# Performance work log

Measured on AMD Instinct MI355X. Metric: run time of the kernel, lower is better.

The kernel has to match this reference:

```python
import jax, jax.numpy as jnp
import numpy as np

B, T, D, H = 4, 2048, 1024, 16
HD = D // H  # 64


def setup_inputs() -> dict:
    key = jax.random.key(0)
    ks = jax.random.split(key, 5)
    return {
        "x": jax.random.normal(ks[0], (B, T, D), dtype=jnp.float32),
        "W_qkv": jax.random.normal(ks[1], (D, 3 * D), dtype=jnp.float32) * 0.02,
        "b_qkv": jax.random.normal(ks[2], (3 * D,), dtype=jnp.float32) * 0.02,
        "W_out": jax.random.normal(ks[3], (D, D), dtype=jnp.float32) * 0.02,
        "b_out": jax.random.normal(ks[4], (D,), dtype=jnp.float32) * 0.02,
        "mask": 1,
    }


def reference(x, W_qkv, b_qkv, W_out, b_out, mask):
    # fused QKV projection: (B,T,3D)
    qkv = x @ W_qkv + b_qkv
    # torch layout: view (B,T,H,3*hd) then chunk last dim into q,k,v
    qkv = qkv.reshape(B, T, H, 3, HD)
    q = qkv[..., 0, :].transpose(0, 2, 1, 3)  # (B,H,T,hd)
    k = qkv[..., 1, :].transpose(0, 2, 1, 3)
    v = qkv[..., 2, :].transpose(0, 2, 1, 3)
    scores = jnp.einsum('bhqd,bhkd->bhqk', q, k) / jnp.sqrt(jnp.float32(HD))
    if mask:
        causal = jnp.triu(jnp.ones((T, T), dtype=bool), k=1)
        scores = jnp.where(causal[None, None], jnp.float32(-jnp.inf), scores)
    attn = jax.nn.softmax(scores, axis=-1)
    out = jnp.einsum('bhqk,bhkd->bhqd', attn, v)  # (B,H,T,hd)
    out = out.transpose(0, 2, 1, 3).reshape(B, T, D)
    return out @ W_out + b_out
```

## Files before the change

### kernel.cpp

```cpp
#include <hip/hip_runtime.h>

typedef unsigned short u16;
typedef __bf16 bf16x8 __attribute__((ext_vector_type(8)));
typedef float f32x4 __attribute__((ext_vector_type(4)));
typedef float f32x16 __attribute__((ext_vector_type(16)));

#define DEV __device__ __forceinline__

constexpr int Bb = 4, Tt = 2048, Dd = 1024, Hh = 16, HDd = 64;
constexpr int MM = Bb * Tt;
constexpr float QSCALE = 0.125f * 1.4426950408889634f;

DEV u16 f2bf(float f) {
  unsigned u = __float_as_uint(f);
  u += 0x7fffu + ((u >> 16) & 1u);
  return (u16)(u >> 16);
}

DEV unsigned cvtpk(float a, float b) {
  unsigned r;
  asm("v_cvt_pk_bf16_f32 %0, %1, %2" : "=v"(r) : "v"(a), "v"(b));
  return r;
}

DEV void pswap(unsigned& a, unsigned& b) {
  asm("v_permlane32_swap_b32 %0, %1" : "+v"(a), "+v"(b));
}

DEV void gload_lds16(const u16* g, u16* l) {
  __builtin_amdgcn_global_load_lds(
      (const __attribute__((address_space(1))) void*)g,
      (__attribute__((address_space(3))) void*)l, 16, 0, 0);
}

__global__ __launch_bounds__(256) void cast_x_kernel(const float* __restrict__ in,
                                                     u16* __restrict__ out, int n8) {
  int i = blockIdx.x * 256 + threadIdx.x;
  if (i >= n8) return;
  const float4* p = (const float4*)in + (size_t)i * 2;
  float4 v0 = p[0], v1 = p[1];
  union { u16 u[8]; uint4 v; } t;
  t.u[0] = f2bf(v0.x); t.u[1] = f2bf(v0.y); t.u[2] = f2bf(v0.z); t.u[3] = f2bf(v0.w);
  t.u[4] = f2bf(v1.x); t.u[5] = f2bf(v1.y); t.u[6] = f2bf(v1.z); t.u[7] = f2bf(v1.w);
  ((uint4*)out)[i] = t.v;
}

__global__ __launch_bounds__(256) void wcast_t_kernel(const float* __restrict__ in,
                                                      u16* __restrict__ out, int K, int N) {
  __shared__ float tile[32][33];
  int n0 = blockIdx.x * 32, k0 = blockIdx.y * 32;
  int tx = threadIdx.x & 31, ty = threadIdx.x >> 5;
  #pragma unroll
  for (int yy = ty; yy < 32; yy += 8)
    tile[yy][tx] = in[(size_t)(k0 + yy) * N + n0 + tx];
  __syncthreads();
  #pragma unroll
  for (int yy = ty; yy < 32; yy += 8)
    out[(size_t)(n0 + yy) * K + k0 + tx] = f2bf(tile[tx][yy]);
}

DEV void stage_tile(const u16* __restrict__ src, int row0, int k0, int ld, u16* lds) {
  int t = threadIdx.x, w = t >> 6;
  #pragma unroll
  for (int j = 0; j < 2; ++j) {
    int e = (j * 256 + t) * 8;
    int r = e >> 5;
    int slot = (e >> 3) & 3;
    int c = (slot ^ ((r >> 1) & 3)) << 3;
    gload_lds16(src + (size_t)(row0 + r) * ld + k0 + c, lds + j * 2048 + w * 512);
  }
}

template <int EPI>
__global__ __launch_bounds__(256) void gemm_bt_kernel(
    const u16* __restrict__ A, const u16* __restrict__ Bt,
    const float* __restrict__ bias, float* __restrict__ Cf,
    u16* __restrict__ Qb, u16* __restrict__ Kb, u16* __restrict__ Vtb,
    int M, int N, int Kd) {
  __shared__ __align__(16) u16 SH[24576];
  int nx = N >> 7;
  int bid = blockIdx.y * nx + blockIdx.x;
  int nwg = (M >> 7) * nx;
  int swz = (bid & 7) * (nwg >> 3) + (bid >> 3);
  int m0 = (swz / nx) * 128, n0 = (swz % nx) * 128;

  int tid = threadIdx.x, l = tid & 63, w = tid >> 6;
  int lo = l & 15, g = l >> 4;
  int wm = (w >> 1) * 64, wn = (w & 1) * 64;
  f32x4 acc[4][4] = {};
  int nk = Kd >> 5;
  stage_tile(A, m0, 0, Kd, SH);
  stage_tile(Bt, n0, 0, Kd, SH + 12288);
  stage_tile(A, m0, 32, Kd, SH + 4096);
  stage_tile(Bt, n0, 32, Kd, SH + 12288 + 4096);
  asm volatile("s_waitcnt vmcnt(4)" ::: "memory");
  __builtin_amdgcn_s_barrier();
  for (int kt = 0; kt < nk; ++kt) {
    if (kt + 2 < nk) {
      int bi = (kt + 2) % 3;
      stage_tile(A, m0, (kt + 2) * 32, Kd, SH + bi * 4096);
      stage_tile(Bt, n0, (kt + 2) * 32, Kd, SH + 12288 + bi * 4096);
    }
    const u16* Ac = SH + (kt % 3) * 4096;
    const u16* Bc = SH + 12288 + (kt % 3) * 4096;
    bf16x8 a[4], b[4];
    #pragma unroll
    for (int i = 0; i < 4; ++i) {
      int row = wm + i * 16 + lo;
      a[i] = *(const bf16x8*)&Ac[row * 32 + ((g ^ ((row >> 1) & 3)) << 3)];
    }
    #pragma unroll
    for (int j = 0; j < 4; ++j) {
      int row = wn + j * 16 + lo;
      b[j] = *(const bf16x8*)&Bc[row * 32 + ((g ^ ((row >> 1) & 3)) << 3)];
    }
    #pragma unroll
    for (int i = 0; i < 4; ++i)
      #pragma unroll
      for (int j = 0; j < 4; ++j)
        acc[i][j] = __builtin_amdgcn_mfma_f32_16x16x32_bf16(a[i], b[j], acc[i][j], 0, 0, 0);
    if (kt + 2 < nk) {
      asm volatile("s_waitcnt vmcnt(4)" ::: "memory");
    } else {
      asm volatile("s_waitcnt vmcnt(0)" ::: "memory");
    }
    __builtin_amdgcn_s_barrier();
  }
  if (EPI == 0) {
    u16* ep = SH + w * 4096;
    int nblk = n0 + wn;
    int hh = nblk / 192, which = (nblk % 192) >> 6;
    int mblk = m0 + wm;
    int b_ = mblk >> 11, t0 = mblk & (Tt - 1);
    if (which == 2) {
      #pragma unroll
      for (int j = 0; j < 4; ++j) {
        float bv = bias[nblk + j * 16 + lo];
        int rowp = j * 16 + lo;
        #pragma unroll
        for (int i = 0; i < 4; ++i) {
          int slotp = i * 2 + (g >> 1);
          #pragma unroll
          for (int r = 0; r < 4; ++r) {
            ep[rowp * 64 + ((slotp ^ (rowp & 7)) << 3) + (g & 1) * 4 + r] =
                f2bf(acc[i][j][r] + bv);
          }
        }
      }
      asm volatile("s_waitcnt lgkmcnt(0)" ::: "memory");
      u16* dst = Vtb + (size_t)(b_ * Hh + hh) * HDd * Tt + t0;
      #pragma unroll
      for (int s = 0; s < 8; ++s) {
        int row = s * 8 + (l >> 3);
        int phys = ((l & 7) ^ (row & 7)) << 3;
        uint4 v = *(const uint4*)&ep[row * 64 + phys];
        *(uint4*)(dst + (size_t)row * Tt + (l & 7) * 8) = v;
      }
    } else {
      float qs = (which == 0) ? QSCALE : 1.0f;
      #pragma unroll
      for (int j = 0; j < 4; ++j) {
        float bv = bias[nblk + j * 16 + lo];
        int slot = j * 2 + (lo >> 3);
        #pragma unroll
        for (int i = 0; i < 4; ++i) {
          #pragma unroll
          for (int r = 0; r < 4; ++r) {
            int lrow = i * 16 + g * 4 + r;
            ep[lrow * 64 + ((slot ^ (lrow & 7)) << 3) + (lo & 7)] =
                f2bf((acc[i][j][r] + bv) * qs);
          }
        }
      }
      asm volatile("s_waitcnt lgkmcnt(0)" ::: "memory");
      u16* dst = (which == 0) ? Qb : Kb;
      dst += ((size_t)(b_ * Hh + hh) * Tt + t0) * HDd;
      #pragma unroll
      for (int s = 0; s < 8; ++s) {
        int row = s * 8 + (l >> 3);
        int phys = ((l & 7) ^ (row & 7)) << 3;
        uint4 v = *(const uint4*)&ep[row * 64 + phys];
        *(uint4*)(dst + row * 64 + (l & 7) * 8) = v;
      }
    }
  } else {
    #pragma unroll
    for (int j = 0; j < 4; ++j) {
      int n = n0 + wn + j * 16 + lo;
      float bv = bias[n];
      #pragma unroll
      for (int i = 0; i < 4; ++i) {
        #pragma unroll
        for (int r = 0; r < 4; ++r) {
          int m = m0 + wm + i * 16 + g * 4 + r;
          Cf[(size_t)m * N + n] = acc[i][j][r] + bv;
        }
      }
    }
  }
}

DEV void stage512(const u16* __restrict__ g, size_t rstride, u16* lds) {
  int t = threadIdx.x;
  int r = t >> 3, pp = t & 7;
  int lg = pp ^ (r & 7);
  gload_lds16(g + (size_t)r * rstride + lg * 8, lds + (size_t)(t & ~63) * 8);
}

DEV void build_pfrags(const f32x16& s, bf16x8& f0, bf16x8& f1) {
  unsigned w0 = cvtpk(s[0], s[1]),  w1 = cvtpk(s[2], s[3]);
  unsigned w2 = cvtpk(s[4], s[5]),  w3 = cvtpk(s[6], s[7]);
  unsigned w4 = cvtpk(s[8], s[9]),  w5 = cvtpk(s[10], s[11]);
  unsigned w6 = cvtpk(s[12], s[13]), w7 = cvtpk(s[14], s[15]);
  pswap(w0, w2);
  pswap(w1, w3);
  pswap(w4, w6);
  pswap(w5, w7);
  union { unsigned u[4]; bf16x8 v; } t0, t1;
  t0.u[0] = w0; t0.u[1] = w1; t0.u[2] = w2; t0.u[3] = w3;
  t1.u[0] = w4; t1.u[1] = w5; t1.u[2] = w6; t1.u[3] = w7;
  f0 = t0.v; f1 = t1.v;
}

DEV void write_o(u16* __restrict__ O, size_t rowbase, const f32x16& o0,
                 const f32x16& o1, float L, int hf) {
  float inv = 1.0f / L;
  #pragma unroll
  for (int m = 0; m < 4; ++m) {
    uint2 v0, v1;
    v0.x = cvtpk(o0[4 * m] * inv,     o0[4 * m + 1] * inv);
    v0.y = cvtpk(o0[4 * m + 2] * inv, o0[4 * m + 3] * inv);
    *(uint2*)(O + rowbase + m * 8 + hf * 4) = v0;
    v1.x = cvtpk(o1[4 * m] * inv,     o1[4 * m + 1] * inv);
    v1.y = cvtpk(o1[4 * m + 2] * inv, o1[4 * m + 3] * inv);
    *(uint2*)(O + rowbase + 32 + m * 8 + hf * 4) = v1;
  }
}

__global__ __launch_bounds__(512) void attn_kernel(const u16* __restrict__ Q,
                                                   const u16* __restrict__ K,
                                                   const u16* __restrict__ Vt,
                                                   u16* __restrict__ O) {
  __shared__ __align__(16) u16 Ks[4][4096];
  __shared__ __align__(16) u16 Vs[4][4096];
  __shared__ float MLs[8][64][2];
  __shared__ float OSs[4][64][8];
  int p = blockIdx.y & 7;
  int bh = ((int)blockIdx.y >> 3) * 8 + (int)blockIdx.x;
  int b_ = bh >> 4, h = bh & 15;
  const u16* Qp = Q + (size_t)bh * Tt * HDd;
  const u16* Kp = K + (size_t)bh * Tt * HDd;
  const u16* Vp = Vt + (size_t)bh * HDd * Tt;
  int tid = threadIdx.x, w = tid >> 6, l = tid & 63;
  int wq = w & 3, grp = w >> 2;
  int lq = l & 31, hf = l >> 5;
  int JA = 15 - p, JB = p;
  int ntA = 2 * JA + 2;
  constexpr int ntT = 34;

  int q0 = 128 * JA + 32 * wq;
  int qrow = q0 + lq;
  int swz = lq & 7;

  bf16x8 aq[4];
  #pragma unroll
  for (int s = 0; s < 4; ++s)
    aq[s] = *(const bf16x8*)(Qp + (size_t)qrow * HDd + s * 16 + hf * 8);

  f32x16 o0 = {}, o1 = {};
  float M = -1e30f, L = 0.f;

  stage512(Kp, HDd, Ks[0]);
  stage512(Vp, Tt, Vs[0]);
  stage512(Kp + (size_t)64 * HDd, HDd, Ks[1]);
  stage512(Vp + 64, Tt, Vs[1]);
  asm volatile("s_waitcnt vmcnt(0)" ::: "memory");
  __builtin_amdgcn_s_barrier();

  int jB = ntA >> 1;
  for (int j = 0; j < ntT / 2; ++j) {
    int t2 = 2 * j + 2;
    if (t2 < ntT) {
      int kt2 = (t2 < ntA ? t2 : t2 - ntA) * 64;
      stage512(Kp + (size_t)kt2 * HDd, HDd, Ks[t2 & 3]);
      stage512(Vp + kt2, Tt, Vs[t2 & 3]);
      int t3 = t2 + 1;
      int kt3 = (t3 < ntA ? t3 : t3 - ntA) * 64;
      stage512(Kp + (size_t)kt3 * HDd, HDd, Ks[t3 & 3]);
      stage512(Vp + kt3, Tt, Vs[t3 & 3]);
    }
    if (j == jB) {
      MLs[w][l][0] = M; MLs[w][l][1] = L;
      asm volatile("s_waitcnt lgkmcnt(0)" ::: "memory");
      __builtin_amdgcn_s_barrier();
      float Mb = MLs[w ^ 4][l][0], Lb = MLs[w ^ 4][l][1];
      float Mstar = fmaxf(M, Mb);
      float ss = __builtin_amdgcn_exp2f(M - Mstar);
      float sb = __builtin_amdgcn_exp2f(Mb - Mstar);
      float Lm = L * ss + Lb * sb;
      #pragma unroll
      for (int r = 0; r < 16; ++r) { o0[r] *= ss; o1[r] *= ss; }
      #pragma unroll
      for (int c = 0; c < 4; ++c) {
        if (w >= 4) {
          #pragma unroll
          for (int k = 0; k < 8; ++k)
            OSs[wq][l][k] = (c < 2) ? o0[(c & 1) * 8 + k] : o1[(c & 1) * 8 + k];
        }
        asm volatile("s_waitcnt lgkmcnt(0)" ::: "memory");
        __builtin_amdgcn_s_barrier();
        if (w < 4) {
          #pragma unroll
          for (int k = 0; k < 8; ++k) {
            float v = OSs[wq][l][k];
            if (c < 2) o0[(c & 1) * 8 + k] += v; else o1[(c & 1) * 8 + k] += v;
          }
        }
        asm volatile("s_waitcnt lgkmcnt(0)" ::: "memory");
        __builtin_amdgcn_s_barrier();
      }
      if (w < 4) {
        size_t rbA = ((size_t)b_ * Tt + qrow) * Dd + h * HDd;
        write_o(O, rbA, o0, o1, Lm, hf);
      }
      #pragma unroll
      for (int r = 0; r < 16; ++r) { o0[r] = 0.f; o1[r] = 0.f; }
      M = -1e30f; L = 0.f;
      q0 = 128 * JB + 32 * wq;
      qrow = q0 + lq;
      #pragma unroll
      for (int s = 0; s < 4; ++s)
        aq[s] = *(const bf16x8*)(Qp + (size_t)qrow * HDd + s * 16 + hf * 8);
    }
    int myt = 2 * j + grp;
    int kt = (myt < ntA ? myt : myt - ntA) * 64;
    const u16* Kc = Ks[myt & 3];
    const u16* Vc = Vs[myt & 3];
    if (kt < q0 + 32) {
      f32x16 s0 = {}, s1 = {};
      __builtin_amdgcn_s_setprio(1);
      #pragma unroll
      for (int ds = 0; ds < 4; ++ds) {
        int slot = 2 * ds + hf;
        bf16x8 k0 = *(const bf16x8*)&Kc[lq * 64 + ((slot ^ swz) << 3)];
        bf16x8 k1 = *(const bf16x8*)&Kc[(32 + lq) * 64 + ((slot ^ swz) << 3)];
        s0 = __builtin_amdgcn_mfma_f32_32x32x16_bf16(k0, aq[ds], s0, 0, 0, 0);
        s1 = __builtin_amdgcn_mfma_f32_32x32x16_bf16(k1, aq[ds], s1, 0, 0, 0);
      }
      __builtin_amdgcn_s_setprio(0);
      if (kt + 63 > q0) {
        #pragma unroll
        for (int r = 0; r < 16; ++r) {
          int kg = kt + (r & 3) + 8 * (r >> 2) + 4 * hf;
          if (kg > qrow)      s0[r] = -INFINITY;
          if (kg + 32 > qrow) s1[r] = -INFINITY;
        }
      }
      float mx_[16];
      #pragma unroll
      for (int r = 0; r < 16; ++r) mx_[r] = fmaxf(s0[r], s1[r]);
      #pragma unroll
      for (int st = 8; st >= 1; st >>= 1)
        #pragma unroll
        for (int r = 0; r < 16; ++r) if (r < st) mx_[r] = fmaxf(mx_[r], mx_[r + st]);
      float mx = fmaxf(mx_[0], __shfl_xor(mx_[0], 32));
      float sc = 1.f;
      if (!__all(mx <= M + 8.f)) {
        float Mn = fmaxf(M, mx);
        sc = __builtin_amdgcn_exp2f(M - Mn);
        M = Mn;
        #pragma unroll
        for (int r = 0; r < 16; ++r) { o0[r] *= sc; o1[r] *= sc; }
      }
      #pragma unroll
      for (int r = 0; r < 16; ++r) {
        s0[r] = __builtin_amdgcn_exp2f(s0[r] - M);
        s1[r] = __builtin_amdgcn_exp2f(s1[r] - M);
      }
      float ls_[16];
      #pragma unroll
      for (int r = 0; r < 16; ++r) ls_[r] = s0[r] + s1[r];
      #pragma unroll
      for (int st = 8; st >= 1; st >>= 1)
        #pragma unroll
        for (int r = 0; r < 16; ++r) if (r < st) ls_[r] += ls_[r + st];
      float ls = ls_[0] + __shfl_xor(ls_[0], 32);
      L = L * sc + ls;
      bf16x8 pf0, pf1, pf2, pf3;
      build_pfrags(s0, pf0, pf1);
      build_pfrags(s1, pf2, pf3);
      __builtin_amdgcn_s_setprio(1);
      #pragma unroll
      for (int ks = 0; ks < 4; ++ks) {
        int slot = 2 * ks + hf;
        bf16x8 v0 = *(const bf16x8*)&Vc[lq * 64 + ((slot ^ swz) << 3)];
        bf16x8 v1 = *(const bf16x8*)&Vc[(32 + lq) * 64 + ((slot ^ swz) << 3)];
        bf16x8 pf = (ks == 0) ? pf0 : (ks == 1) ? pf1 : (ks == 2) ? pf2 : pf3;
        o0 = __builtin_amdgcn_mfma_f32_32x32x16_bf16(v0, pf, o0, 0, 0, 0);
        o1 = __builtin_amdgcn_mfma_f32_32x32x16_bf16(v1, pf, o1, 0, 0, 0);
      }
      __builtin_amdgcn_s_setprio(0);
    }
    asm volatile("s_waitcnt vmcnt(0)" ::: "memory");
    __builtin_amdgcn_s_barrier();
  }

  MLs[w][l][0] = M; MLs[w][l][1] = L;
  asm volatile("s_waitcnt lgkmcnt(0)" ::: "memory");
  __builtin_amdgcn_s_barrier();
  float Mb = MLs[w ^ 4][l][0], Lb = MLs[w ^ 4][l][1];
  float Mstar = fmaxf(M, Mb);
  float ss = __builtin_amdgcn_exp2f(M - Mstar);
  float sb = __builtin_amdgcn_exp2f(Mb - Mstar);
  float Lm = L * ss + Lb * sb;
  #pragma unroll
  for (int r = 0; r < 16; ++r) { o0[r] *= ss; o1[r] *= ss; }
  #pragma unroll
  for (int c = 0; c < 4; ++c) {
    if (w >= 4) {
      #pragma unroll
      for (int k = 0; k < 8; ++k)
        OSs[wq][l][k] = (c < 2) ? o0[(c & 1) * 8 + k] : o1[(c & 1) * 8 + k];
    }
    asm volatile("s_waitcnt lgkmcnt(0)" ::: "memory");
    __builtin_amdgcn_s_barrier();
    if (w < 4) {
      #pragma unroll
      for (int k = 0; k < 8; ++k) {
        float v = OSs[wq][l][k];
        if (c < 2) o0[(c & 1) * 8 + k] += v; else o1[(c & 1) * 8 + k] += v;
      }
    }
    asm volatile("s_waitcnt lgkmcnt(0)" ::: "memory");
    __builtin_amdgcn_s_barrier();
  }
  if (w < 4) {
    size_t rbB = ((size_t)b_ * Tt + qrow) * Dd + h * HDd;
    write_o(O, rbB, o0, o1, Lm, hf);
  }
}

extern "C" void kernel_launch(void* const* d_in, const int* in_sizes, int n_in,
                              void* d_out, int out_size, void* d_ws, size_t ws_size,
                              hipStream_t stream) {
  const float* x    = (const float*)d_in[0];
  const float* Wqkv = (const float*)d_in[1];
  const float* bqkv = (const float*)d_in[2];
  const float* Wout = (const float*)d_in[3];
  const float* bout = (const float*)d_in[4];
  float* out = (float*)d_out;
  char* ws = (char*)d_ws;

  u16* xb    = (u16*)(ws + 0);
  u16* Ob    = (u16*)(ws + 0);
  u16* Wqkvt = (u16*)(ws + 16777216);
  u16* Woutt = (u16*)(ws + 23068672);
  u16* Qb    = (u16*)(ws + 25165824);
  u16* Kb    = (u16*)(ws + 41943040);
  u16* Vtb   = (u16*)(ws + 58720256);

  cast_x_kernel<<<4096, 256, 0, stream>>>(x, xb, (MM * Dd) / 8);
  wcast_t_kernel<<<dim3(96, 32), 256, 0, stream>>>(Wqkv, Wqkvt, Dd, 3 * Dd);
  wcast_t_kernel<<<dim3(32, 32), 256, 0, stream>>>(Wout, Woutt, Dd, Dd);
  gemm_bt_kernel<0><<<dim3(24, 64), 256, 0, stream>>>(
      xb, Wqkvt, bqkv, nullptr, Qb, Kb, Vtb, MM, 3 * Dd, Dd);
  attn_kernel<<<dim3(8, 64), 512, 0, stream>>>(Qb, Kb, Vtb, Ob);
  gemm_bt_kernel<1><<<dim3(8, 64), 256, 0, stream>>>(
      Ob, Woutt, bout, out, nullptr, nullptr, nullptr, MM, Dd, Dd);
}
```

Measured before the change: 179.4 us.

## Use 256x256-tile GEMM with 32x32 MFMA for QKV projection

Replaces the 128x128 QKV projection GEMM with a dedicated 256x256-tile kernel of 512 threads. It uses 32x32x16 bf16 MFMAs, a triple-buffered LDS pipeline and raised wave priority around the MFMA block. The epilogue is rewritten to scatter the 32x32 accumulator layout into the Q, K and transposed V buffers. Larger tiles cut global and LDS traffic per flop, at the cost of only 384 workgroups, which may underfill the GPU, plus higher register and LDS pressure.

Result: slower. 185.7 us (+3.5%).

```diff
diff --git a/kernel.cpp b/kernel.cpp
--- a/kernel.cpp
+++ b/kernel.cpp
@@ -59,6 +59,157 @@
     out[(size_t)(n0 + yy) * K + k0 + tx] = f2bf(tile[tx][yy]);
 }
 
+DEV void stage256(const u16* __restrict__ src, int row0, int k0, int ld, u16* lds) {
+  int t = threadIdx.x;
+  #pragma unroll
+  for (int j = 0; j < 2; ++j) {
+    int e = j * 512 + t;
+    int r = e >> 2, slot = e & 3;
+    int c = (slot ^ ((r >> 1) & 3)) << 3;
+    gload_lds16(src + (size_t)(row0 + r) * ld + k0 + c,
+                lds + (size_t)(j * 512 + (t & ~63)) * 8);
+  }
+}
+
+__global__ __launch_bounds__(512, 2) void gemm256_qkv_kernel(
+    const u16* __restrict__ A, const u16* __restrict__ Bt,
+    const float* __restrict__ bias,
+    u16* __restrict__ Qb, u16* __restrict__ Kb, u16* __restrict__ Vtb,
+    int M, int N, int Kd) {
+  __shared__ __align__(16) u16 SH[49152];
+  int nx = N >> 8;
+  int bid = blockIdx.y * nx + blockIdx.x;
+  int nwg = (M >> 8) * nx;
+  int swz = (bid & 7) * (nwg >> 3) + (bid >> 3);
+  int m0 = (swz / nx) * 256, n0 = (swz % nx) * 256;
+
+  int tid = threadIdx.x, l = tid & 63, w = tid >> 6;
+  int lq = l & 31, hf = l >> 5;
+  int wr = w >> 2, wc = w & 3;
+  f32x16 acc[4][2] = {};
+  int nk = Kd >> 5;
+  stage256(A, m0, 0, Kd, SH);
+  stage256(Bt, n0, 0, Kd, SH + 24576);
+  stage256(A, m0, 32, Kd, SH + 8192);
+  stage256(Bt, n0, 32, Kd, SH + 24576 + 8192);
+  asm volatile("s_waitcnt vmcnt(4)" ::: "memory");
+  __builtin_amdgcn_s_barrier();
+  for (int kt = 0; kt < nk; ++kt) {
+    if (kt + 2 < nk) {
+      int bi = (kt + 2) % 3;
+      stage256(A, m0, (kt + 2) * 32, Kd, SH + bi * 8192);
+      stage256(Bt, n0, (kt + 2) * 32, Kd, SH + 24576 + bi * 8192);
+    }
+    const u16* Ac = SH + (kt % 3) * 8192;
+    const u16* Bc = SH + 24576 + (kt % 3) * 8192;
+    bf16x8 a[4][2], b[2][2];
+    #pragma unroll
+    for (int rb = 0; rb < 4; ++rb)
+      #pragma unroll
+      for (int ks = 0; ks < 2; ++ks) {
+        int row = wr * 128 + rb * 32 + lq;
+        int s = ks * 2 + hf;
+        a[rb][ks] = *(const bf16x8*)&Ac[row * 32 + ((s ^ ((row >> 1) & 3)) << 3)];
+      }
+    #pragma unroll
+    for (int cb = 0; cb < 2; ++cb)
+      #pragma unroll
+      for (int ks = 0; ks < 2; ++ks) {
+        int row = wc * 64 + cb * 32 + lq;
+        int s = ks * 2 + hf;
+        b[cb][ks] = *(const bf16x8*)&Bc[row * 32 + ((s ^ ((row >> 1) & 3)) << 3)];
+      }
+    __builtin_amdgcn_s_setprio(1);
+    #pragma unroll
+    for (int rb = 0; rb < 4; ++rb)
+      #pragma unroll
+      for (int cb = 0; cb < 2; ++cb)
+        #pragma unroll
+        for (int ks = 0; ks < 2; ++ks)
+          acc[rb][cb] = __builtin_amdgcn_mfma_f32_32x32x16_bf16(
+              a[rb][ks], b[cb][ks], acc[rb][cb], 0, 0, 0);
+    __builtin_amdgcn_s_setprio(0);
+    if (kt + 2 < nk) {
+      asm volatile("s_waitcnt vmcnt(4)" ::: "memory");
+    } else {
+      asm volatile("s_waitcnt vmcnt(0)" ::: "memory");
+    }
+    __builtin_amdgcn_s_barrier();
+  }
+  u16* ep = SH + w * 4096;
+  int nblk = n0 + wc * 64;
+  int hh = nblk / 192, seg = (nblk % 192) >> 6;
+  int mbase = m0 + wr * 128;
+  int b_ = mbase >> 11;
+  float bv0 = bias[nblk + lq];
+  float bv1 = bias[nblk + 32 + lq];
+  if (seg == 2) {
+    u16* dst0 = Vtb + (size_t)(b_ * Hh + hh) * HDd * Tt;
+    #pragma unroll
+    for (int rh = 0; rh < 2; ++rh) {
+      #pragma unroll
+      for (int cb = 0; cb < 2; ++cb) {
+        float bv = cb ? bv1 : bv0;
+        int prow = cb * 32 + lq;
+        #pragma unroll
+        for (int rr = 0; rr < 2; ++rr) {
+          int rb = 2 * rh + rr;
+          #pragma unroll
+          for (int g16 = 0; g16 < 16; ++g16) {
+            int pcol = rr * 32 + (g16 & 3) + 8 * (g16 >> 2) + 4 * hf;
+            int slot = pcol >> 3;
+            ep[prow * 64 + ((slot ^ (prow & 7)) << 3) + (pcol & 7)] =
+                f2bf(acc[rb][cb][g16] + bv);
+          }
+        }
+      }
+      asm volatile("s_waitcnt lgkmcnt(0)" ::: "memory");
+      int t0 = (mbase + rh * 64) & (Tt - 1);
+      #pragma unroll
+      for (int s = 0; s < 8; ++s) {
+        int row = s * 8 + (l >> 3);
+        int phys = ((l & 7) ^ (row & 7)) << 3;
+        uint4 v = *(const uint4*)&ep[row * 64 + phys];
+        *(uint4*)(dst0 + (size_t)row * Tt + t0 + (l & 7) * 8) = v;
+      }
+      asm volatile("s_waitcnt lgkmcnt(0)" ::: "memory");
+    }
+  } else {
+    float qs = (seg == 0) ? QSCALE : 1.0f;
+    u16* dstbase = ((seg == 0) ? Qb : Kb) + (size_t)(b_ * Hh + hh) * Tt * HDd;
+    #pragma unroll
+    for (int rh = 0; rh < 2; ++rh) {
+      #pragma unroll
+      for (int rr = 0; rr < 2; ++rr) {
+        int rb = 2 * rh + rr;
+        #pragma unroll
+        for (int cb = 0; cb < 2; ++cb) {
+          float bv = cb ? bv1 : bv0;
+          int pcol = cb * 32 + lq;
+          int slot = pcol >> 3;
+          #pragma unroll
+          for (int g16 = 0; g16 < 16; ++g16) {
+            int prow = rr * 32 + (g16 & 3) + 8 * (g16 >> 2) + 4 * hf;
+            ep[prow * 64 + ((slot ^ (prow & 7)) << 3) + (pcol & 7)] =
+                f2bf((acc[rb][cb][g16] + bv) * qs);
+          }
+        }
+      }
+      asm volatile("s_waitcnt lgkmcnt(0)" ::: "memory");
+      int t0 = (mbase + rh * 64) & (Tt - 1);
+      u16* dst = dstbase + (size_t)t0 * HDd;
+      #pragma unroll
+      for (int s = 0; s < 8; ++s) {
+        int row = s * 8 + (l >> 3);
+        int phys = ((l & 7) ^ (row & 7)) << 3;
+        uint4 v = *(const uint4*)&ep[row * 64 + phys];
+        *(uint4*)(dst + row * 64 + (l & 7) * 8) = v;
+      }
+      asm volatile("s_waitcnt lgkmcnt(0)" ::: "memory");
+    }
+  }
+}
+
 DEV void stage_tile(const u16* __restrict__ src, int row0, int k0, int ld, u16* lds) {
   int t = threadIdx.x, w = t >> 6;
   #pragma unroll
@@ -71,11 +222,9 @@
   }
 }
 
-template <int EPI>
-__global__ __launch_bounds__(256) void gemm_bt_kernel(
+__global__ __launch_bounds__(256) void gemm_out_kernel(
     const u16* __restrict__ A, const u16* __restrict__ Bt,
     const float* __restrict__ bias, float* __restrict__ Cf,
-    u16* __restrict__ Qb, u16* __restrict__ Kb, u16* __restrict__ Vtb,
     int M, int N, int Kd) {
   __shared__ __align__(16) u16 SH[24576];
   int nx = N >> 7;
@@ -126,75 +275,16 @@
     }
     __builtin_amdgcn_s_barrier();
   }
-  if (EPI == 0) {
-    u16* ep = SH + w * 4096;
-    int nblk = n0 + wn;
-    int hh = nblk / 192, which = (nblk % 192) >> 6;
-    int mblk = m0 + wm;
-    int b_ = mblk >> 11, t0 = mblk & (Tt - 1);
-    if (which == 2) {
-      #pragma unroll
-      for (int j = 0; j < 4; ++j) {
-        float bv = bias[nblk + j * 16 + lo];
-        int rowp = j * 16 + lo;
-        #pragma unroll
-        for (int i = 0; i < 4; ++i) {
-          int slotp = i * 2 + (g >> 1);
-          #pragma unroll
-          for (int r = 0; r < 4; ++r) {
-            ep[rowp * 64 + ((slotp ^ (rowp & 7)) << 3) + (g & 1) * 4 + r] =
-                f2bf(acc[i][j][r] + bv);
-          }
-        }
-      }
-      asm volatile("s_waitcnt lgkmcnt(0)" ::: "memory");
-      u16* dst = Vtb + (size_t)(b_ * Hh + hh) * HDd * Tt + t0;
-      #pragma unroll
-      for (int s = 0; s < 8; ++s) {
-        int row = s * 8 + (l >> 3);
-        int phys = ((l & 7) ^ (row & 7)) << 3;
-        uint4 v = *(const uint4*)&ep[row * 64 + phys];
-        *(uint4*)(dst + (size_t)row * Tt + (l & 7) * 8) = v;
-      }
-    } else {
-      float qs = (which == 0) ? QSCALE : 1.0f;
-      #pragma unroll
-      for (int j = 0; j < 4; ++j) {
-        float bv = bias[nblk + j * 16 + lo];
-        int slot = j * 2 + (lo >> 3);
-        #pragma unroll
-        for (int i = 0; i < 4; ++i) {
-          #pragma unroll
-          for (int r = 0; r < 4; ++r) {
-            int lrow = i * 16 + g * 4 + r;
-            ep[lrow * 64 + ((slot ^ (lrow & 7)) << 3) + (lo & 7)] =
-                f2bf((acc[i][j][r] + bv) * qs);
-          }
-        }
-      }
-      asm volatile("s_waitcnt lgkmcnt(0)" ::: "memory");
-      u16* dst = (which == 0) ? Qb : Kb;
-      dst += ((size_t)(b_ * Hh + hh) * Tt + t0) * HDd;
-      #pragma unroll
-      for (int s = 0; s < 8; ++s) {
-        int row = s * 8 + (l >> 3);
-        int phys = ((l & 7) ^ (row & 7)) << 3;
-        uint4 v = *(const uint4*)&ep[row * 64 + phys];
-        *(uint4*)(dst + row * 64 + (l & 7) * 8) = v;
-      }
-    }
-  } else {
-    #pragma unroll
-    for (int j = 0; j < 4; ++j) {
-      int n = n0 + wn + j * 16 + lo;
-      float bv = bias[n];
-      #pragma unroll
-      for (int i = 0; i < 4; ++i) {
-        #pragma unroll
-        for (int r = 0; r < 4; ++r) {
-          int m = m0 + wm + i * 16 + g * 4 + r;
-          Cf[(size_t)m * N + n] = acc[i][j][r] + bv;
-        }
+  #pragma unroll
+  for (int j = 0; j < 4; ++j) {
+    int n = n0 + wn + j * 16 + lo;
+    float bv = bias[n];
+    #pragma unroll
+    for (int i = 0; i < 4; ++i) {
+      #pragma unroll
+      for (int r = 0; r < 4; ++r) {
+        int m = m0 + wm + i * 16 + g * 4 + r;
+        Cf[(size_t)m * N + n] = acc[i][j][r] + bv;
       }
     }
   }
@@ -462,9 +552,9 @@
   cast_x_kernel<<<4096, 256, 0, stream>>>(x, xb, (MM * Dd) / 8);
   wcast_t_kernel<<<dim3(96, 32), 256, 0, stream>>>(Wqkv, Wqkvt, Dd, 3 * Dd);
   wcast_t_kernel<<<dim3(32, 32), 256, 0, stream>>>(Wout, Woutt, Dd, Dd);
-  gemm_bt_kernel<0><<<dim3(24, 64), 256, 0, stream>>>(
-      xb, Wqkvt, bqkv, nullptr, Qb, Kb, Vtb, MM, 3 * Dd, Dd);
+  gemm256_qkv_kernel<<<dim3(12, 32), 512, 0, stream>>>(
+      xb, Wqkvt, bqkv, Qb, Kb, Vtb, MM, 3 * Dd, Dd);
   attn_kernel<<<dim3(8, 64), 512, 0, stream>>>(Qb, Kb, Vtb, Ob);
-  gemm_bt_kernel<1><<<dim3(8, 64), 256, 0, stream>>>(
-      Ob, Woutt, bout, out, nullptr, nullptr, nullptr, MM, Dd, Dd);
-}
+  gemm_out_kernel<<<dim3(8, 64), 256, 0, stream>>>(
+      Ob, Woutt, bout, out, MM, Dd, Dd);
+}
```

## Use 128x256 tiles with 8 waves for the QKV projection GEMM

Applied to the files above, without the earlier changes.

Adds a dedicated QKV GEMM kernel that uses 512-thread workgroups computing 128x256 output tiles, so each A tile is reused across twice as many columns and the grid halves. It also raises MFMA issue priority around the inner product and runs the LDS-staged epilogue in two rounds because LDS only holds four wave scratch buffers at once. The output projection GEMM is split out as its own non-templated kernel. The risks are the larger LDS footprint (72KB), which limits occupancy, and the serialized epilogue rounds.

Measured after the change: 172.4 us (median of 3 runs). 3.9% less time.

```diff
diff --git a/kernel.cpp b/kernel.cpp
--- a/kernel.cpp
+++ b/kernel.cpp
@@ -59,6 +59,144 @@
     out[(size_t)(n0 + yy) * K + k0 + tx] = f2bf(tile[tx][yy]);
 }
 
+DEV void stageA128(const u16* __restrict__ src, int row0, int k0, int ld, u16* lds) {
+  int t = threadIdx.x;
+  int r = t >> 2, slot = t & 3;
+  int c = (slot ^ ((r >> 1) & 3)) << 3;
+  gload_lds16(src + (size_t)(row0 + r) * ld + k0 + c, lds + (size_t)(t & ~63) * 8);
+}
+DEV void stageB256(const u16* __restrict__ src, int row0, int k0, int ld, u16* lds) {
+  int t = threadIdx.x;
+  #pragma unroll
+  for (int j = 0; j < 2; ++j) {
+    int e = j * 512 + t;
+    int r = e >> 2, slot = e & 3;
+    int c = (slot ^ ((r >> 1) & 3)) << 3;
+    gload_lds16(src + (size_t)(row0 + r) * ld + k0 + c,
+                lds + (size_t)(j * 512 + (t & ~63)) * 8);
+  }
+}
+
+__global__ __launch_bounds__(512, 4) void gemm_qkv_kernel(
+    const u16* __restrict__ A, const u16* __restrict__ Bt,
+    const float* __restrict__ bias,
+    u16* __restrict__ Qb, u16* __restrict__ Kb, u16* __restrict__ Vtb,
+    int M, int N, int Kd) {
+  __shared__ __align__(16) u16 SH[36864];
+  int nx = N >> 8;
+  int bid = blockIdx.y * nx + blockIdx.x;
+  int nwg = (M >> 7) * nx;
+  int swz = (bid & 7) * (nwg >> 3) + (bid >> 3);
+  int m0 = (swz / nx) * 128, n0 = (swz % nx) * 256;
+
+  int tid = threadIdx.x, l = tid & 63, w = tid >> 6;
+  int lo = l & 15, g = l >> 4;
+  int wm = (w >> 2) * 64, wn = (w & 3) * 64;
+  f32x4 acc[4][4] = {};
+  int nk = Kd >> 5;
+  stageA128(A, m0, 0, Kd, SH);
+  stageB256(Bt, n0, 0, Kd, SH + 12288);
+  stageA128(A, m0, 32, Kd, SH + 4096);
+  stageB256(Bt, n0, 32, Kd, SH + 12288 + 8192);
+  asm volatile("s_waitcnt vmcnt(3)" ::: "memory");
+  __builtin_amdgcn_s_barrier();
+  for (int kt = 0; kt < nk; ++kt) {
+    if (kt + 2 < nk) {
+      int bi = (kt + 2) % 3;
+      stageA128(A, m0, (kt + 2) * 32, Kd, SH + bi * 4096);
+      stageB256(Bt, n0, (kt + 2) * 32, Kd, SH + 12288 + bi * 8192);
+    }
+    const u16* Ac = SH + (kt % 3) * 4096;
+    const u16* Bc = SH + 12288 + (kt % 3) * 8192;
+    bf16x8 a[4], b[4];
+    #pragma unroll
+    for (int i = 0; i < 4; ++i) {
+      int row = wm + i * 16 + lo;
+      a[i] = *(const bf16x8*)&Ac[row * 32 + ((g ^ ((row >> 1) & 3)) << 3)];
+    }
+    #pragma unroll
+    for (int j = 0; j < 4; ++j) {
+      int row = wn + j * 16 + lo;
+      b[j] = *(const bf16x8*)&Bc[row * 32 + ((g ^ ((row >> 1) & 3)) << 3)];
+    }
+    __builtin_amdgcn_s_setprio(1);
+    #pragma unroll
+    for (int i = 0; i < 4; ++i)
+      #pragma unroll
+      for (int j = 0; j < 4; ++j)
+        acc[i][j] = __builtin_amdgcn_mfma_f32_16x16x32_bf16(a[i], b[j], acc[i][j], 0, 0, 0);
+    __builtin_amdgcn_s_setprio(0);
+    if (kt + 2 < nk) {
+      asm volatile("s_waitcnt vmcnt(3)" ::: "memory");
+    } else {
+      asm volatile("s_waitcnt vmcnt(0)" ::: "memory");
+    }
+    __builtin_amdgcn_s_barrier();
+  }
+  #pragma unroll
+  for (int round = 0; round < 2; ++round) {
+    if ((w >> 2) == round) {
+      u16* ep = SH + (w & 3) * 4096;
+      int nblk = n0 + wn;
+      int hh = nblk / 192, which = (nblk % 192) >> 6;
+      int mblk = m0 + wm;
+      int b_ = mblk >> 11, t0 = mblk & (Tt - 1);
+      if (which == 2) {
+        #pragma unroll
+        for (int j = 0; j < 4; ++j) {
+          float bv = bias[nblk + j * 16 + lo];
+          int rowp = j * 16 + lo;
+          #pragma unroll
+          for (int i = 0; i < 4; ++i) {
+            int slotp = i * 2 + (g >> 1);
+            #pragma unroll
+            for (int r = 0; r < 4; ++r) {
+              ep[rowp * 64 + ((slotp ^ (rowp & 7)) << 3) + (g & 1) * 4 + r] =
+                  f2bf(acc[i][j][r] + bv);
+            }
+          }
+        }
+        asm volatile("s_waitcnt lgkmcnt(0)" ::: "memory");
+        u16* dst = Vtb + (size_t)(b_ * Hh + hh) * HDd * Tt + t0;
+        #pragma unroll
+        for (int s = 0; s < 8; ++s) {
+          int row = s * 8 + (l >> 3);
+          int phys = ((l & 7) ^ (row & 7)) << 3;
+          uint4 v = *(const uint4*)&ep[row * 64 + phys];
+          *(uint4*)(dst + (size_t)row * Tt + (l & 7) * 8) = v;
+        }
+      } else {
+        float qs = (which == 0) ? QSCALE : 1.0f;
+        #pragma unroll
+        for (int j = 0; j < 4; ++j) {
+          float bv = bias[nblk + j * 16 + lo];
+          int slot = j * 2 + (lo >> 3);
+          #pragma unroll
+          for (int i = 0; i < 4; ++i) {
+            #pragma unroll
+            for (int r = 0; r < 4; ++r) {
+              int lrow = i * 16 + g * 4 + r;
+              ep[lrow * 64 + ((slot ^ (lrow & 7)) << 3) + (lo & 7)] =
+                  f2bf((acc[i][j][r] + bv) * qs);
+            }
+          }
+        }
+        asm volatile("s_waitcnt lgkmcnt(0)" ::: "memory");
+        u16* dst = (which == 0) ? Qb : Kb;
+        dst += ((size_t)(b_ * Hh + hh) * Tt + t0) * HDd;
+        #pragma unroll
+        for (int s = 0; s < 8; ++s) {
+          int row = s * 8 + (l >> 3);
+          int phys = ((l & 7) ^ (row & 7)) << 3;
+          uint4 v = *(const uint4*)&ep[row * 64 + phys];
+          *(uint4*)(dst + row * 64 + (l & 7) * 8) = v;
+        }
+      }
+    }
+    __syncthreads();
+  }
+}
+
 DEV void stage_tile(const u16* __restrict__ src, int row0, int k0, int ld, u16* lds) {
   int t = threadIdx.x, w = t >> 6;
   #pragma unroll
@@ -71,11 +209,9 @@
   }
 }
 
-template <int EPI>
-__global__ __launch_bounds__(256) void gemm_bt_kernel(
+__global__ __launch_bounds__(256) void gemm_out_kernel(
     const u16* __restrict__ A, const u16* __restrict__ Bt,
     const float* __restrict__ bias, float* __restrict__ Cf,
-    u16* __restrict__ Qb, u16* __restrict__ Kb, u16* __restrict__ Vtb,
     int M, int N, int Kd) {
   __shared__ __align__(16) u16 SH[24576];
   int nx = N >> 7;
@@ -126,75 +262,16 @@
     }
     __builtin_amdgcn_s_barrier();
   }
-  if (EPI == 0) {
-    u16* ep = SH + w * 4096;
-    int nblk = n0 + wn;
-    int hh = nblk / 192, which = (nblk % 192) >> 6;
-    int mblk = m0 + wm;
-    int b_ = mblk >> 11, t0 = mblk & (Tt - 1);
-    if (which == 2) {
-      #pragma unroll
-      for (int j = 0; j < 4; ++j) {
-        float bv = bias[nblk + j * 16 + lo];
-        int rowp = j * 16 + lo;
-        #pragma unroll
-        for (int i = 0; i < 4; ++i) {
-          int slotp = i * 2 + (g >> 1);
-          #pragma unroll
-          for (int r = 0; r < 4; ++r) {
-            ep[rowp * 64 + ((slotp ^ (rowp & 7)) << 3) + (g & 1) * 4 + r] =
-                f2bf(acc[i][j][r] + bv);
-          }
-        }
-      }
-      asm volatile("s_waitcnt lgkmcnt(0)" ::: "memory");
-      u16* dst = Vtb + (size_t)(b_ * Hh + hh) * HDd * Tt + t0;
-      #pragma unroll
-      for (int s = 0; s < 8; ++s) {
-        int row = s * 8 + (l >> 3);
-        int phys = ((l & 7) ^ (row & 7)) << 3;
-        uint4 v = *(const uint4*)&ep[row * 64 + phys];
-        *(uint4*)(dst + (size_t)row * Tt + (l & 7) * 8) = v;
-      }
-    } else {
-      float qs = (which == 0) ? QSCALE : 1.0f;
-      #pragma unroll
-      for (int j = 0; j < 4; ++j) {
-        float bv = bias[nblk + j * 16 + lo];
-        int slot = j * 2 + (lo >> 3);
-        #pragma unroll
-        for (int i = 0; i < 4; ++i) {
-          #pragma unroll
-          for (int r = 0; r < 4; ++r) {
-            int lrow = i * 16 + g * 4 + r;
-            ep[lrow * 64 + ((slot ^ (lrow & 7)) << 3) + (lo & 7)] =
-                f2bf((acc[i][j][r] + bv) * qs);
-          }
-        }
-      }
-      asm volatile("s_waitcnt lgkmcnt(0)" ::: "memory");
-      u16* dst = (which == 0) ? Qb : Kb;
-      dst += ((size_t)(b_ * Hh + hh) * Tt + t0) * HDd;
-      #pragma unroll
-      for (int s = 0; s < 8; ++s) {
-        int row = s * 8 + (l >> 3);
-        int phys = ((l & 7) ^ (row & 7)) << 3;
-        uint4 v = *(const uint4*)&ep[row * 64 + phys];
-        *(uint4*)(dst + row * 64 + (l & 7) * 8) = v;
-      }
-    }
-  } else {
-    #pragma unroll
-    for (int j = 0; j < 4; ++j) {
-      int n = n0 + wn + j * 16 + lo;
-      float bv = bias[n];
-      #pragma unroll
-      for (int i = 0; i < 4; ++i) {
-        #pragma unroll
-        for (int r = 0; r < 4; ++r) {
-          int m = m0 + wm + i * 16 + g * 4 + r;
-          Cf[(size_t)m * N + n] = acc[i][j][r] + bv;
-        }
+  #pragma unroll
+  for (int j = 0; j < 4; ++j) {
+    int n = n0 + wn + j * 16 + lo;
+    float bv = bias[n];
+    #pragma unroll
+    for (int i = 0; i < 4; ++i) {
+      #pragma unroll
+      for (int r = 0; r < 4; ++r) {
+        int m = m0 + wm + i * 16 + g * 4 + r;
+        Cf[(size_t)m * N + n] = acc[i][j][r] + bv;
       }
     }
   }
@@ -462,9 +539,9 @@
   cast_x_kernel<<<4096, 256, 0, stream>>>(x, xb, (MM * Dd) / 8);
   wcast_t_kernel<<<dim3(96, 32), 256, 0, stream>>>(Wqkv, Wqkvt, Dd, 3 * Dd);
   wcast_t_kernel<<<dim3(32, 32), 256, 0, stream>>>(Wout, Woutt, Dd, Dd);
-  gemm_bt_kernel<0><<<dim3(24, 64), 256, 0, stream>>>(
-      xb, Wqkvt, bqkv, nullptr, Qb, Kb, Vtb, MM, 3 * Dd, Dd);
+  gemm_qkv_kernel<<<dim3(12, 64), 512, 0, stream>>>(
+      xb, Wqkvt, bqkv, Qb, Kb, Vtb, MM, 3 * Dd, Dd);
   attn_kernel<<<dim3(8, 64), 512, 0, stream>>>(Qb, Kb, Vtb, Ob);
-  gemm_bt_kernel<1><<<dim3(8, 64), 256, 0, stream>>>(
-      Ob, Woutt, bout, out, nullptr, nullptr, nullptr, MM, Dd, Dd);
-}
+  gemm_out_kernel<<<dim3(8, 64), 256, 0, stream>>>(
+      Ob, Woutt, bout, out, MM, Dd, Dd);
+}
```
